# Kernel optimization log

Hardware: AMD Instinct MI355X
Metric: run time of the kernel (lower is better)

Reference implementation:

```python
import jax, jax.numpy as jnp
import numpy as np
import math

B, TT, TS, C, H, L = 8, 256, 512, 512, 8, 10
HD = C // H
TOPK_FRAME = 64
# layer schedule mirrors MultimodalTransformer.forward tower order:
# 4 stimulus cross-attn (kv=frames, topk), 2 causal self-attn, 2 history cross-attn, 2 causal self-attn
# kv_source: 0=frames, 1=self, 2=id_prev
SCHED = [(0, False, TOPK_FRAME)] * 4 + [(1, True, None)] * 2 + [(2, False, None)] * 2 + [(1, True, None)] * 2


def setup_inputs() -> dict:
    key = jax.random.key(0)
    ks = jax.random.split(key, 4)
    kws = jax.random.split(ks[3], 6)
    w = lambda k, s: jax.random.normal(k, s, jnp.float32) * 0.02
    return {
        "id_x": jax.random.normal(ks[0], (B, TT, C), jnp.float32),
        "id_prev": jax.random.normal(ks[1], (B, TT, C), jnp.float32),
        "frames": jax.random.normal(ks[2], (B, TS, C), jnp.float32),
        "Wq": w(kws[0], (L, C, C)), "bq": jnp.zeros((L, C), jnp.float32),
        "Wk": w(kws[1], (L, C, C)), "bk": jnp.zeros((L, C), jnp.float32),
        "Wv": w(kws[2], (L, C, C)), "bv": jnp.zeros((L, C), jnp.float32),
        "Wo": w(kws[3], (L, C, C)), "bo": jnp.zeros((L, C), jnp.float32),
        "W1": w(kws[4], (L, C, 4 * C)), "b1": jnp.zeros((L, 4 * C), jnp.float32),
        "W2": w(kws[5], (L, 4 * C, C)), "b2": jnp.zeros((L, C), jnp.float32),
        "ln1_g": jnp.ones((L, C), jnp.float32), "ln1_b": jnp.zeros((L, C), jnp.float32),
        "ln2_g": jnp.ones((L, C), jnp.float32), "ln2_b": jnp.zeros((L, C), jnp.float32),
        "lnf_g": jnp.ones((L, C), jnp.float32), "lnf_b": jnp.zeros((L, C), jnp.float32),
    }


def _ln(x, g, b):
    mu = x.mean(-1, keepdims=True)
    var = ((x - mu) ** 2).mean(-1, keepdims=True)
    return (x - mu) * jax.lax.rsqrt(var + 1e-5) * g + b


def _block(x, kv, causal, topk, p):
    # Block.forward: x = x + attn(ln1(x), kv, kv, mask); x = x + mlp(ln2(x)); return ln_f(x)
    Wq, bq, Wk, bk, Wv, bv, Wo, bo, W1, b1, W2, b2, l1g, l1b, l2g, l2b, lfg, lfb = p
    Bx, Tt, Cx = x.shape
    Ts = kv.shape[1]
    h = _ln(x, l1g, l1b)
    q = (h @ Wq + bq).reshape(Bx, Tt, H, HD).transpose(0, 2, 1, 3)   # [B,H,Tt,HD]
    k = (kv @ Wk + bk).reshape(Bx, Ts, H, HD).transpose(0, 2, 1, 3)  # [B,H,Ts,HD]
    v = (kv @ Wv + bv).reshape(Bx, Ts, H, HD).transpose(0, 2, 1, 3)
    att = jnp.einsum('bhqd,bhkd->bhqk', q, k) * (1.0 / math.sqrt(HD))
    if causal:
        m = jnp.tril(jnp.ones((Tt, Ts), dtype=bool))
        att = jnp.where(m, att, -jnp.inf)
    if topk is not None and topk < Ts:
        top = jax.lax.top_k(att, topk)[0]           # [B,H,Tt,topk]
        att = jnp.where(att < top[..., -1:], -jnp.inf, att)
    w_att = jax.nn.softmax(att, axis=-1)
    y = jnp.einsum('bhqk,bhkd->bhqd', w_att, v).transpose(0, 2, 1, 3).reshape(Bx, Tt, Cx)
    x = x + y @ Wo + bo
    h2 = _ln(x, l2g, l2b)
    x = x + jax.nn.gelu(h2 @ W1 + b1, approximate=False) @ W2 + b2
    return _ln(x, lfg, lfb)


def _forward(id_x, id_prev, frames, Wq, bq, Wk, bk, Wv, bv, Wo, bo, W1, b1, W2, b2,
             ln1_g, ln1_b, ln2_g, ln2_b, lnf_g, lnf_b):
    x = id_x
    for i, (src, causal, topk) in enumerate(SCHED):
        kv = (frames, x, id_prev)[src]
        p = (Wq[i], bq[i], Wk[i], bk[i], Wv[i], bv[i], Wo[i], bo[i],
             W1[i], b1[i], W2[i], b2[i],
             ln1_g[i], ln1_b[i], ln2_g[i], ln2_b[i], lnf_g[i], lnf_b[i])
        x = _block(x, kv, causal, topk, p)
    return x


def reference(id_x, id_prev, frames, Wq, bq, Wk, bk, Wv, bv, Wo, bo, W1, b1, W2, b2,
              ln1_g, ln1_b, ln2_g, ln2_b, lnf_g, lnf_b):
    return _forward(id_x, id_prev, frames, Wq, bq, Wk, bk, Wv, bv, Wo, bo, W1, b1, W2, b2,
                    ln1_g, ln1_b, ln2_g, ln2_b, lnf_g, lnf_b)
```

## Files before the change

kernel.cpp:

```cpp
#include <hip/hip_runtime.h>
#include <math.h>

#define CC 512
#define NH 8
#define HD 64
#define TT 256

typedef __attribute__((ext_vector_type(8))) short short8v;
typedef __attribute__((ext_vector_type(4))) float f32x4;

__device__ inline unsigned short bfc(float f) {
  unsigned u = __float_as_uint(f);
  return (unsigned short)((u + 0x7fffu + ((u >> 16) & 1u)) >> 16);
}
__device__ inline float b2f(unsigned short s) {
  return __uint_as_float((unsigned)s << 16);
}

__global__ __launch_bounds__(256) void prep_k(const float* __restrict__ id_x,
    const float* __restrict__ frames, const float* __restrict__ id_prev,
    float* __restrict__ x, unsigned short* __restrict__ fb,
    unsigned short* __restrict__ pb) {
  int i = blockIdx.x * 256 + threadIdx.x;
  if (i < 262144) {
    ((float4*)x)[i] = ((const float4*)id_x)[i];
  } else if (i < 786432) {
    int j = i - 262144;
    float4 f = ((const float4*)frames)[j];
    ushort4 o; o.x = bfc(f.x); o.y = bfc(f.y); o.z = bfc(f.z); o.w = bfc(f.w);
    ((ushort4*)fb)[j] = o;
  } else {
    int j = i - 786432;
    float4 f = ((const float4*)id_prev)[j];
    ushort4 o; o.x = bfc(f.x); o.y = bfc(f.y); o.z = bfc(f.z); o.w = bfc(f.w);
    ((ushort4*)pb)[j] = o;
  }
}

__global__ __launch_bounds__(256) void ln_bf(const float* __restrict__ in,
    unsigned short* __restrict__ out, const float* __restrict__ g, const float* __restrict__ b) {
  int row = blockIdx.x, t = threadIdx.x;
  const float* r = in + (size_t)row * CC;
  float v0 = r[t], v1 = r[t + 256];
  float s = v0 + v1;
  #pragma unroll
  for (int o = 32; o; o >>= 1) s += __shfl_xor(s, o);
  __shared__ float r1[4], r2[4];
  if ((t & 63) == 0) r1[t >> 6] = s;
  __syncthreads();
  float mu = (r1[0] + r1[1] + r1[2] + r1[3]) * (1.0f / CC);
  float d0 = v0 - mu, d1 = v1 - mu;
  float sq = d0 * d0 + d1 * d1;
  #pragma unroll
  for (int o = 32; o; o >>= 1) sq += __shfl_xor(sq, o);
  if ((t & 63) == 0) r2[t >> 6] = sq;
  __syncthreads();
  float inv = rsqrtf((r2[0] + r2[1] + r2[2] + r2[3]) * (1.0f / CC) + 1e-5f);
  out[(size_t)row * CC + t]       = bfc(d0 * inv * g[t] + b[t]);
  out[(size_t)row * CC + t + 256] = bfc(d1 * inv * g[t + 256] + b[t + 256]);
}

__global__ __launch_bounds__(256) void ln_final(const float* __restrict__ in,
    float* __restrict__ out, const float* __restrict__ g, const float* __restrict__ b) {
  int row = blockIdx.x, t = threadIdx.x;
  const float* r = in + (size_t)row * CC;
  float v0 = r[t], v1 = r[t + 256];
  float s = v0 + v1;
  #pragma unroll
  for (int o = 32; o; o >>= 1) s += __shfl_xor(s, o);
  __shared__ float r1[4], r2[4];
  if ((t & 63) == 0) r1[t >> 6] = s;
  __syncthreads();
  float mu = (r1[0] + r1[1] + r1[2] + r1[3]) * (1.0f / CC);
  float d0 = v0 - mu, d1 = v1 - mu;
  float sq = d0 * d0 + d1 * d1;
  #pragma unroll
  for (int o = 32; o; o >>= 1) sq += __shfl_xor(sq, o);
  if ((t & 63) == 0) r2[t >> 6] = sq;
  __syncthreads();
  float inv = rsqrtf((r2[0] + r2[1] + r2[2] + r2[3]) * (1.0f / CC) + 1e-5f);
  out[(size_t)row * CC + t]       = d0 * inv * g[t] + b[t];
  out[(size_t)row * CC + t + 256] = d1 * inv * g[t + 256] + b[t + 256];
}

__global__ __launch_bounds__(256) void ln_chain(const float* __restrict__ in,
    float* __restrict__ xout, unsigned short* __restrict__ xb,
    const float* __restrict__ gf, const float* __restrict__ bf,
    const float* __restrict__ g1, const float* __restrict__ b1,
    unsigned short* __restrict__ hout) {
  int row = blockIdx.x, t = threadIdx.x;
  const float* r = in + (size_t)row * CC;
  float v0 = r[t], v1 = r[t + 256];
  float s = v0 + v1;
  #pragma unroll
  for (int o = 32; o; o >>= 1) s += __shfl_xor(s, o);
  __shared__ float r1[4], r2[4];
  if ((t & 63) == 0) r1[t >> 6] = s;
  __syncthreads();
  float mu = (r1[0] + r1[1] + r1[2] + r1[3]) * (1.0f / CC);
  float d0 = v0 - mu, d1 = v1 - mu;
  float sq = d0 * d0 + d1 * d1;
  #pragma unroll
  for (int o = 32; o; o >>= 1) sq += __shfl_xor(sq, o);
  if ((t & 63) == 0) r2[t >> 6] = sq;
  __syncthreads();
  float inv = rsqrtf((r2[0] + r2[1] + r2[2] + r2[3]) * (1.0f / CC) + 1e-5f);
  float xf0 = d0 * inv * gf[t] + bf[t];
  float xf1 = d1 * inv * gf[t + 256] + bf[t + 256];
  xout[(size_t)row * CC + t]       = xf0;
  xout[(size_t)row * CC + t + 256] = xf1;
  xb[(size_t)row * CC + t]         = bfc(xf0);
  xb[(size_t)row * CC + t + 256]   = bfc(xf1);
  __syncthreads();
  float s2 = xf0 + xf1;
  #pragma unroll
  for (int o = 32; o; o >>= 1) s2 += __shfl_xor(s2, o);
  if ((t & 63) == 0) r1[t >> 6] = s2;
  __syncthreads();
  float mu2 = (r1[0] + r1[1] + r1[2] + r1[3]) * (1.0f / CC);
  float e0 = xf0 - mu2, e1 = xf1 - mu2;
  float sq2 = e0 * e0 + e1 * e1;
  #pragma unroll
  for (int o = 32; o; o >>= 1) sq2 += __shfl_xor(sq2, o);
  if ((t & 63) == 0) r2[t >> 6] = sq2;
  __syncthreads();
  float inv2 = rsqrtf((r2[0] + r2[1] + r2[2] + r2[3]) * (1.0f / CC) + 1e-5f);
  hout[(size_t)row * CC + t]       = bfc(e0 * inv2 * g1[t] + b1[t]);
  hout[(size_t)row * CC + t + 256] = bfc(e1 * inv2 * g1[t + 256] + b1[t + 256]);
}

__global__ __launch_bounds__(256) void transpose_w(
    const float* __restrict__ Wq, const float* __restrict__ Wk,
    const float* __restrict__ Wv, const float* __restrict__ Wo,
    const float* __restrict__ W1, const float* __restrict__ W2,
    int layer_base, unsigned short* __restrict__ wT) {
  int lz = blockIdx.x / 3072;
  int layer = layer_base + lz;
  int bid = blockIdx.x - lz * 3072;
  unsigned short* wTl = wT + (size_t)lz * 3145728;
  const float* src; unsigned short* dst; int R, Cn, tile, lg;
  if (bid < 1024) {
    int seg = bid >> 8; tile = bid & 255; R = 512; Cn = 512; lg = 4;
    const float* s4[4] = {Wq, Wk, Wv, Wo};
    src = s4[seg] + (size_t)layer * 262144;
    dst = wTl + (size_t)seg * 262144;
  } else if (bid < 2048) {
    tile = bid - 1024; R = 512; Cn = 2048; lg = 6;
    src = W1 + (size_t)layer * 1048576; dst = wTl + 1048576;
  } else {
    tile = bid - 2048; R = 2048; Cn = 512; lg = 4;
    src = W2 + (size_t)layer * 1048576; dst = wTl + 2097152;
  }
  int trb = tile >> lg, tcb = tile & ((1 << lg) - 1);
  __shared__ float tl[32][33];
  int t = threadIdx.x;
  int r = t >> 3, c4 = (t & 7) << 2;
  const float* sp = src + (size_t)(trb * 32 + r) * Cn + tcb * 32 + c4;
  float4 fv = *(const float4*)sp;
  tl[r][c4] = fv.x; tl[r][c4 + 1] = fv.y; tl[r][c4 + 2] = fv.z; tl[r][c4 + 3] = fv.w;
  __syncthreads();
  unsigned short* dp = dst + (size_t)(tcb * 32 + r) * R + trb * 32 + c4;
  ushort4 ov;
  ov.x = bfc(tl[c4][r]); ov.y = bfc(tl[c4 + 1][r]);
  ov.z = bfc(tl[c4 + 2][r]); ov.w = bfc(tl[c4 + 3][r]);
  *(ushort4*)dp = ov;
}

template<int BM, int GELU, int RES, int OUTBF, int BIAS2>
__global__ __launch_bounds__(256) void gemm_bf(
    const unsigned short* __restrict__ A, const unsigned short* __restrict__ WT,
    const float* __restrict__ bias, const float* __restrict__ bias2,
    void* __restrict__ outp, const float* __restrict__ res, int M, int N, int K) {
  __shared__ unsigned short As[BM * 64];
  __shared__ unsigned short Bs[64 * 64];
  const int tid = threadIdx.x, lane = tid & 63, wid = tid >> 6;
  const int bm = blockIdx.y * BM, bn = blockIdx.x << 6;
  const int wm = (wid >> 1) * (BM / 2), wn = (wid & 1) << 5;
  constexpr int MF = BM / 32;
  f32x4 acc[MF][2] = {};
  const int fr = lane & 15, fq = lane >> 4;
  for (int k0 = 0; k0 < K; k0 += 64) {
    if (k0) __syncthreads();
    #pragma unroll
    for (int i = 0; i < BM / 32; i++) {
      int gl = tid + (i << 8);
      int row = gl >> 3, gc = gl & 7;
      short8v d = *(const short8v*)(A + (size_t)(bm + row) * K + k0 + (gc << 3));
      *(short8v*)((char*)As + ((((row << 7) + (gc << 4))) ^ ((row & 7) << 4))) = d;
    }
    #pragma unroll
    for (int i = 0; i < 2; i++) {
      int gl = tid + (i << 8);
      int row = gl >> 3, gc = gl & 7;
      short8v d = *(const short8v*)(WT + (size_t)(bn + row) * K + k0 + (gc << 3));
      *(short8v*)((char*)Bs + ((((row << 7) + (gc << 4))) ^ ((row & 7) << 4))) = d;
    }
    __syncthreads();
    short8v af[MF][2], bf2[2][2];
    #pragma unroll
    for (int mf = 0; mf < MF; mf++)
      #pragma unroll
      for (int ks = 0; ks < 2; ks++) {
        int r = wm + mf * 16 + fr;
        int c = (ks << 2) + fq;
        af[mf][ks] = *(const short8v*)((const char*)As + ((((r << 7) + (c << 4))) ^ ((r & 7) << 4)));
      }
    #pragma unroll
    for (int nf = 0; nf < 2; nf++)
      #pragma unroll
      for (int ks = 0; ks < 2; ks++) {
        int r = wn + nf * 16 + fr;
        int c = (ks << 2) + fq;
        bf2[nf][ks] = *(const short8v*)((const char*)Bs + ((((r << 7) + (c << 4))) ^ ((r & 7) << 4)));
      }
    #pragma unroll
    for (int mf = 0; mf < MF; mf++)
      #pragma unroll
      for (int nf = 0; nf < 2; nf++) {
        acc[mf][nf] = __builtin_amdgcn_mfma_f32_16x16x32_bf16(af[mf][0], bf2[nf][0], acc[mf][nf], 0, 0, 0);
        acc[mf][nf] = __builtin_amdgcn_mfma_f32_16x16x32_bf16(af[mf][1], bf2[nf][1], acc[mf][nf], 0, 0, 0);
      }
  }
  #pragma unroll
  for (int mf = 0; mf < MF; mf++)
    #pragma unroll
    for (int nf = 0; nf < 2; nf++) {
      int col = bn + wn + nf * 16 + fr;
      float bia = (BIAS2 && col >= 512) ? bias2[col - 512] : bias[col];
      #pragma unroll
      for (int rr = 0; rr < 4; rr++) {
        int row = bm + wm + mf * 16 + fq * 4 + rr;
        float vv = acc[mf][nf][rr] + bia;
        if (GELU) vv = 0.5f * vv * (1.0f + erff(vv * 0.70710678118654752f));
        if (RES)  vv += res[(size_t)row * N + col];
        if (OUTBF) ((unsigned short*)outp)[(size_t)row * N + col] = bfc(vv);
        else       ((float*)outp)[(size_t)row * N + col] = vv;
      }
    }
}

template<int CAUSAL, int TOPK, int TSK>
__global__ __launch_bounds__(256, 5) void attn_m(
    const float* __restrict__ qf, const unsigned short* __restrict__ kv,
    unsigned short* __restrict__ yb) {
  constexpr int NT = TSK / 64;
  constexpr int NKC = TSK / 128;
  constexpr int SST = TSK + 8;
  __shared__ float S[4 * SST];
  __shared__ unsigned short Ks[128 * 64];
  __shared__ unsigned short Qs[16 * 64];
  __shared__ float swt[TOPK ? 4 : 1][TOPK ? 128 : 1];
  __shared__ unsigned short kidx[TOPK ? 4 : 1][TOPK ? 128 : 1];
  int tid = threadIdx.x, lane = tid & 63, wid = tid >> 6;
  int bid = blockIdx.x;
  int swz = ((bid & 7) << 9) | (bid >> 3);
  int b = swz >> 9, h = (swz >> 6) & 7, qt = swz & 63;
  int q0 = qt << 2;
  {
    int row = tid >> 4, c4 = (tid & 15) << 2;
    ushort4 o;
    if (row < 4) {
      float4 qv = *(const float4*)(qf + (size_t)((b << 8) + q0 + row) * CC + (h << 6) + c4);
      o.x = bfc(qv.x * 0.125f); o.y = bfc(qv.y * 0.125f);
      o.z = bfc(qv.z * 0.125f); o.w = bfc(qv.w * 0.125f);
    } else {
      o.x = o.y = o.z = o.w = 0;
    }
    int off = (row << 7) + (c4 << 1);
    *(ushort4*)((char*)Qs + (off ^ ((row & 7) << 4))) = o;
  }
  __syncthreads();
  short8v aF[2];
  {
    int r = lane & 15, kq = lane >> 4;
    #pragma unroll
    for (int kc2 = 0; kc2 < 2; kc2++)
      aF[kc2] = *(const short8v*)((const char*)Qs +
                 (((r << 7) + (kc2 << 6) + (kq << 4)) ^ ((r & 7) << 4)));
  }
  int nte = NKC;
  if (CAUSAL) { int ub = (q0 + 4 + 127) >> 7; nte = ub < NKC ? ub : NKC; }
  const unsigned short* kgb = kv + (size_t)b * TSK * 1024 + (h << 6);
  for (int t = 0; t < nte; t++) {
    __syncthreads();
    {
      int row = tid & 127, seg = tid >> 7;
      const unsigned short* src = kgb + (size_t)((t << 7) + row) * 1024 + (seg << 5);
      #pragma unroll
      for (int j = 0; j < 4; j++) {
        short8v d = *(const short8v*)(src + (j << 3));
        int slot = (seg << 2) + j;
        *(short8v*)((char*)Ks + (((row << 7) + (slot << 4)) ^ ((row & 7) << 4))) = d;
      }
    }
    __syncthreads();
    int kq = lane >> 4;
    #pragma unroll
    for (int f = 0; f < 2; f++) {
      f32x4 acc = {};
      int key16 = (wid << 5) + (f << 4) + (lane & 15);
      #pragma unroll
      for (int kc2 = 0; kc2 < 2; kc2++) {
        short8v bF = *(const short8v*)((const char*)Ks +
                      (((key16 << 7) + (kc2 << 6) + (kq << 4)) ^ ((key16 & 7) << 4)));
        acc = __builtin_amdgcn_mfma_f32_16x16x32_bf16(aF[kc2], bF, acc, 0, 0, 0);
      }
      if (kq == 0) {
        int col = (t << 7) + key16;
        #pragma unroll
        for (int r = 0; r < 4; r++)
          S[r * SST + col] = acc[r];
      }
    }
  }
  __syncthreads();
  int row = wid;
  int qi = q0 + row;
  int jmax = CAUSAL ? (qi + 1) : TSK;
  const unsigned short* vgb = kv + (size_t)b * TSK * 1024 + 512 + (h << 6) + lane;
  float sc[NT];
  float lmax = -3.0e38f;
  #pragma unroll
  for (int tt = 0; tt < NT; tt++) {
    int key = lane + (tt << 6);
    float v = (!CAUSAL || key < jmax) ? S[row * SST + key] : -3.0e38f;
    sc[tt] = v;
    lmax = fmaxf(lmax, v);
  }
  float mx = lmax;
  #pragma unroll
  for (int o = 32; o; o >>= 1) mx = fmaxf(mx, __shfl_xor(mx, o));
  float oacc = 0.f;
  if (TOPK) {
    unsigned key[NT];
    #pragma unroll
    for (int tt = 0; tt < NT; tt++) {
      unsigned u = __float_as_uint(sc[tt]);
      key[tt] = (u & 0x80000000u) ? ~u : (u | 0x80000000u);
    }
    unsigned prefix = 0u;
    #pragma unroll
    for (int bit = 31; bit >= 0; bit--) {
      unsigned cand = prefix | (1u << bit);
      int cnt = 0;
      #pragma unroll
      for (int tt = 0; tt < NT; tt++)
        cnt += __popcll(__ballot(key[tt] >= cand));
      if (cnt >= 64) prefix = cand;
    }
    float wvv[NT];
    float psum = 0.f;
    int basec = 0;
    #pragma unroll
    for (int tt = 0; tt < NT; tt++) {
      bool keep = key[tt] >= prefix;
      float wv = keep ? exp2f((sc[tt] - mx) * 1.4426950408889634f) : 0.f;
      wvv[tt] = wv;
      psum += wv;
      unsigned long long mask = __ballot(keep);
      if (keep) {
        int pos = basec + (int)__popcll(mask & ((1ull << lane) - 1ull));
        if (pos < 128) {
          kidx[row][pos] = (unsigned short)(lane + (tt << 6));
          swt[row][pos] = wv;
        }
      }
      basec += (int)__popcll(mask);
    }
    #pragma unroll
    for (int o = 32; o; o >>= 1) psum += __shfl_xor(psum, o);
    float inv = 1.0f / psum;
    int nk = basec;
    if (nk <= 128) {
      float a0 = 0.f, a1 = 0.f, a2 = 0.f, a3 = 0.f;
      int i = 0;
      for (; i + 3 < nk; i += 4) {
        a0 += swt[row][i]     * b2f(vgb[(size_t)kidx[row][i] * 1024]);
        a1 += swt[row][i + 1] * b2f(vgb[(size_t)kidx[row][i + 1] * 1024]);
        a2 += swt[row][i + 2] * b2f(vgb[(size_t)kidx[row][i + 2] * 1024]);
        a3 += swt[row][i + 3] * b2f(vgb[(size_t)kidx[row][i + 3] * 1024]);
      }
      for (; i < nk; i++) a0 += swt[row][i] * b2f(vgb[(size_t)kidx[row][i] * 1024]);
      oacc = (a0 + a1 + a2 + a3) * inv;
    } else {
      #pragma unroll
      for (int tt = 0; tt < NT; tt++)
        S[row * SST + lane + (tt << 6)] = wvv[tt];
      float a0 = 0.f, a1 = 0.f;
      for (int j = 0; j + 1 < TSK; j += 2) {
        a0 += S[row * SST + j]     * b2f(vgb[(size_t)j * 1024]);
        a1 += S[row * SST + j + 1] * b2f(vgb[(size_t)(j + 1) * 1024]);
      }
      oacc = (a0 + a1) * inv;
    }
  } else {
    float psum = 0.f;
    #pragma unroll
    for (int tt = 0; tt < NT; tt++) {
      int keyj = lane + (tt << 6);
      float wv = (keyj < jmax) ? exp2f((sc[tt] - mx) * 1.4426950408889634f) : 0.f;
      S[row * SST + keyj] = wv;
      psum += wv;
    }
    #pragma unroll
    for (int o = 32; o; o >>= 1) psum += __shfl_xor(psum, o);
    float inv = 1.0f / psum;
    float a0 = 0.f, a1 = 0.f, a2 = 0.f, a3 = 0.f;
    int j = 0;
    for (; j + 3 < jmax; j += 4) {
      a0 += S[row * SST + j]     * b2f(vgb[(size_t)j * 1024]);
      a1 += S[row * SST + j + 1] * b2f(vgb[(size_t)(j + 1) * 1024]);
      a2 += S[row * SST + j + 2] * b2f(vgb[(size_t)(j + 2) * 1024]);
      a3 += S[row * SST + j + 3] * b2f(vgb[(size_t)(j + 3) * 1024]);
    }
    for (; j < jmax; j++) a0 += S[row * SST + j] * b2f(vgb[(size_t)j * 1024]);
    oacc = (a0 + a1 + a2 + a3) * inv;
  }
  yb[(size_t)((b << 8) + qi) * CC + (h << 6) + lane] = bfc(oacc);
}

extern "C" void kernel_launch(void* const* d_in, const int* in_sizes, int n_in,
                              void* d_out, int out_size, void* d_ws, size_t ws_size,
                              hipStream_t stream) {
  const float* id_x    = (const float*)d_in[0];
  const float* id_prev = (const float*)d_in[1];
  const float* frames  = (const float*)d_in[2];
  const float* Wq = (const float*)d_in[3];  const float* bq = (const float*)d_in[4];
  const float* Wk = (const float*)d_in[5];  const float* bk = (const float*)d_in[6];
  const float* Wv = (const float*)d_in[7];  const float* bv = (const float*)d_in[8];
  const float* Wo = (const float*)d_in[9];  const float* bo = (const float*)d_in[10];
  const float* W1 = (const float*)d_in[11]; const float* b1 = (const float*)d_in[12];
  const float* W2 = (const float*)d_in[13]; const float* b2 = (const float*)d_in[14];
  const float* l1g = (const float*)d_in[15]; const float* l1b = (const float*)d_in[16];
  const float* l2g = (const float*)d_in[17]; const float* l2b = (const float*)d_in[18];
  const float* lfg = (const float*)d_in[19]; const float* lfb = (const float*)d_in[20];

  float* x = (float*)d_out;
  char* W  = (char*)d_ws;
  float*          qfb  = (float*)W;
  unsigned short* kvb  = (unsigned short*)(W + ((size_t)4  << 20));
  unsigned short* m1b  = (unsigned short*)(W + ((size_t)4  << 20));
  unsigned short* hb   = (unsigned short*)(W + ((size_t)12 << 20));
  unsigned short* ybf  = (unsigned short*)(W + ((size_t)14 << 20));
  unsigned short* xb   = (unsigned short*)(W + ((size_t)16 << 20));
  unsigned short* fb   = (unsigned short*)(W + ((size_t)18 << 20));
  unsigned short* pb   = (unsigned short*)(W + ((size_t)22 << 20));
  unsigned short* wT   = (unsigned short*)(W + ((size_t)24 << 20));

  const bool allw = ws_size >= (((size_t)24 << 20) + (size_t)10 * 3145728 * 2);

  prep_k<<<4096, 256, 0, stream>>>(id_x, frames, id_prev, x, fb, pb);
  if (allw)
    transpose_w<<<30720, 256, 0, stream>>>(Wq, Wk, Wv, Wo, W1, W2, 0, wT);

  static const int ssrc[10] = {0, 0, 0, 0, 1, 1, 2, 2, 1, 1};

  for (int i = 0; i < 10; i++) {
    if (!allw)
      transpose_w<<<3072, 256, 0, stream>>>(Wq, Wk, Wv, Wo, W1, W2, i, wT);
    unsigned short* wTl = wT + (allw ? (size_t)i * 3145728 : 0);
    unsigned short* wqT = wTl;
    unsigned short* wkvT = wTl + 262144;
    unsigned short* woT = wTl + 786432;
    unsigned short* w1T = wTl + 1048576;
    unsigned short* w2T = wTl + 2097152;

    if (i == 0)
      ln_bf<<<2048, 256, 0, stream>>>(x, hb, l1g, l1b);

    gemm_bf<32, 0, 0, 0, 0><<<dim3(8, 64), 256, 0, stream>>>(hb, wqT, bq + i * 512, nullptr, qfb, nullptr, 2048, 512, 512);

    const unsigned short* kvsrc; int Mkv;
    if (ssrc[i] == 0)      { kvsrc = fb; Mkv = 4096; }
    else if (ssrc[i] == 1) { kvsrc = xb; Mkv = 2048; }
    else                   { kvsrc = pb; Mkv = 2048; }
    if (Mkv == 4096)
      gemm_bf<64, 0, 0, 1, 1><<<dim3(16, 64), 256, 0, stream>>>(kvsrc, wkvT, bk + i * 512, bv + i * 512, kvb, nullptr, 4096, 1024, 512);
    else
      gemm_bf<32, 0, 0, 1, 1><<<dim3(16, 64), 256, 0, stream>>>(kvsrc, wkvT, bk + i * 512, bv + i * 512, kvb, nullptr, 2048, 1024, 512);

    if (ssrc[i] == 0)      attn_m<0, 1, 512><<<4096, 256, 0, stream>>>(qfb, kvb, ybf);
    else if (ssrc[i] == 1) attn_m<1, 0, 256><<<4096, 256, 0, stream>>>(qfb, kvb, ybf);
    else                   attn_m<0, 0, 256><<<4096, 256, 0, stream>>>(qfb, kvb, ybf);

    gemm_bf<32, 0, 1, 0, 0><<<dim3(8, 64), 256, 0, stream>>>(ybf, woT, bo + i * 512, nullptr, x, x, 2048, 512, 512);
    ln_bf<<<2048, 256, 0, stream>>>(x, hb, l2g + i * 512, l2b + i * 512);
    gemm_bf<64, 1, 0, 1, 0><<<dim3(32, 32), 256, 0, stream>>>(hb, w1T, b1 + i * 2048, nullptr, m1b, nullptr, 2048, 2048, 512);
    gemm_bf<32, 0, 1, 0, 0><<<dim3(8, 64), 256, 0, stream>>>(m1b, w2T, b2 + i * 512, nullptr, x, x, 2048, 512, 2048);

    if (i < 9)
      ln_chain<<<2048, 256, 0, stream>>>(x, x, xb, lfg + i * 512, lfb + i * 512,
                                         l1g + (i + 1) * 512, l1b + (i + 1) * 512, hb);
    else
      ln_final<<<2048, 256, 0, stream>>>(x, x, lfg + i * 512, lfb + i * 512);
  }
}
```

Baseline: 1.187 ms.

## Use direct-to-LDS loads, wave-per-row layernorm, bf16 Q and 8-query attention blocks

LayerNorm kernels now handle one row per wavefront with float4 loads and no shared-memory reductions or barriers. The GEMM and attention K tiles are staged with global_load_lds straight into swizzled LDS instead of going through registers. Q is written as bf16, which halves that buffer's traffic. Attention blocks become 512 threads covering 8 queries, so each K tile load is shared by more queries, and the top-k radix search exits early once exactly 64 candidates are found. These changes touch many kernels at once and risk correctness in the swizzle addressing and in the rewritten attention S-row mapping.

```diff
diff --git a/kernel.cpp b/kernel.cpp
--- a/kernel.cpp
+++ b/kernel.cpp
@@ -15,6 +15,11 @@
 }
 __device__ inline float b2f(unsigned short s) {
   return __uint_as_float((unsigned)s << 16);
+}
+__device__ inline void gld16(const void* g, void* l) {
+  __builtin_amdgcn_global_load_lds(
+      (const __attribute__((address_space(1))) unsigned int*)g,
+      (__attribute__((address_space(3))) unsigned int*)l, 16, 0, 0);
 }
 
 __global__ __launch_bounds__(256) void prep_k(const float* __restrict__ id_x,
@@ -39,48 +44,56 @@
 
 __global__ __launch_bounds__(256) void ln_bf(const float* __restrict__ in,
     unsigned short* __restrict__ out, const float* __restrict__ g, const float* __restrict__ b) {
-  int row = blockIdx.x, t = threadIdx.x;
+  int row = (blockIdx.x << 2) + (threadIdx.x >> 6), lane = threadIdx.x & 63;
   const float* r = in + (size_t)row * CC;
-  float v0 = r[t], v1 = r[t + 256];
-  float s = v0 + v1;
+  float4 v0 = *(const float4*)(r + (lane << 2));
+  float4 v1 = *(const float4*)(r + 256 + (lane << 2));
+  float s = v0.x + v0.y + v0.z + v0.w + v1.x + v1.y + v1.z + v1.w;
   #pragma unroll
   for (int o = 32; o; o >>= 1) s += __shfl_xor(s, o);
-  __shared__ float r1[4], r2[4];
-  if ((t & 63) == 0) r1[t >> 6] = s;
-  __syncthreads();
-  float mu = (r1[0] + r1[1] + r1[2] + r1[3]) * (1.0f / CC);
-  float d0 = v0 - mu, d1 = v1 - mu;
-  float sq = d0 * d0 + d1 * d1;
+  float mu = s * (1.0f / CC);
+  float d0x = v0.x - mu, d0y = v0.y - mu, d0z = v0.z - mu, d0w = v0.w - mu;
+  float d1x = v1.x - mu, d1y = v1.y - mu, d1z = v1.z - mu, d1w = v1.w - mu;
+  float sq = d0x*d0x + d0y*d0y + d0z*d0z + d0w*d0w + d1x*d1x + d1y*d1y + d1z*d1z + d1w*d1w;
   #pragma unroll
   for (int o = 32; o; o >>= 1) sq += __shfl_xor(sq, o);
-  if ((t & 63) == 0) r2[t >> 6] = sq;
-  __syncthreads();
-  float inv = rsqrtf((r2[0] + r2[1] + r2[2] + r2[3]) * (1.0f / CC) + 1e-5f);
-  out[(size_t)row * CC + t]       = bfc(d0 * inv * g[t] + b[t]);
-  out[(size_t)row * CC + t + 256] = bfc(d1 * inv * g[t + 256] + b[t + 256]);
+  float inv = rsqrtf(sq * (1.0f / CC) + 1e-5f);
+  float4 g0 = *(const float4*)(g + (lane << 2)), g1 = *(const float4*)(g + 256 + (lane << 2));
+  float4 b0 = *(const float4*)(b + (lane << 2)), b1 = *(const float4*)(b + 256 + (lane << 2));
+  ushort4 o0, o1;
+  o0.x = bfc(d0x*inv*g0.x + b0.x); o0.y = bfc(d0y*inv*g0.y + b0.y);
+  o0.z = bfc(d0z*inv*g0.z + b0.z); o0.w = bfc(d0w*inv*g0.w + b0.w);
+  o1.x = bfc(d1x*inv*g1.x + b1.x); o1.y = bfc(d1y*inv*g1.y + b1.y);
+  o1.z = bfc(d1z*inv*g1.z + b1.z); o1.w = bfc(d1w*inv*g1.w + b1.w);
+  *(ushort4*)(out + (size_t)row * CC + (lane << 2)) = o0;
+  *(ushort4*)(out + (size_t)row * CC + 256 + (lane << 2)) = o1;
 }
 
 __global__ __launch_bounds__(256) void ln_final(const float* __restrict__ in,
     float* __restrict__ out, const float* __restrict__ g, const float* __restrict__ b) {
-  int row = blockIdx.x, t = threadIdx.x;
+  int row = (blockIdx.x << 2) + (threadIdx.x >> 6), lane = threadIdx.x & 63;
   const float* r = in + (size_t)row * CC;
-  float v0 = r[t], v1 = r[t + 256];
-  float s = v0 + v1;
+  float4 v0 = *(const float4*)(r + (lane << 2));
+  float4 v1 = *(const float4*)(r + 256 + (lane << 2));
+  float s = v0.x + v0.y + v0.z + v0.w + v1.x + v1.y + v1.z + v1.w;
   #pragma unroll
   for (int o = 32; o; o >>= 1) s += __shfl_xor(s, o);
-  __shared__ float r1[4], r2[4];
-  if ((t & 63) == 0) r1[t >> 6] = s;
-  __syncthreads();
-  float mu = (r1[0] + r1[1] + r1[2] + r1[3]) * (1.0f / CC);
-  float d0 = v0 - mu, d1 = v1 - mu;
-  float sq = d0 * d0 + d1 * d1;
+  float mu = s * (1.0f / CC);
+  float d0x = v0.x - mu, d0y = v0.y - mu, d0z = v0.z - mu, d0w = v0.w - mu;
+  float d1x = v1.x - mu, d1y = v1.y - mu, d1z = v1.z - mu, d1w = v1.w - mu;
+  float sq = d0x*d0x + d0y*d0y + d0z*d0z + d0w*d0w + d1x*d1x + d1y*d1y + d1z*d1z + d1w*d1w;
   #pragma unroll
   for (int o = 32; o; o >>= 1) sq += __shfl_xor(sq, o);
-  if ((t & 63) == 0) r2[t >> 6] = sq;
-  __syncthreads();
-  float inv = rsqrtf((r2[0] + r2[1] + r2[2] + r2[3]) * (1.0f / CC) + 1e-5f);
-  out[(size_t)row * CC + t]       = d0 * inv * g[t] + b[t];
-  out[(size_t)row * CC + t + 256] = d1 * inv * g[t + 256] + b[t + 256];
+  float inv = rsqrtf(sq * (1.0f / CC) + 1e-5f);
+  float4 g0 = *(const float4*)(g + (lane << 2)), g1 = *(const float4*)(g + 256 + (lane << 2));
+  float4 b0 = *(const float4*)(b + (lane << 2)), b1 = *(const float4*)(b + 256 + (lane << 2));
+  float4 o0, o1;
+  o0.x = d0x*inv*g0.x + b0.x; o0.y = d0y*inv*g0.y + b0.y;
+  o0.z = d0z*inv*g0.z + b0.z; o0.w = d0w*inv*g0.w + b0.w;
+  o1.x = d1x*inv*g1.x + b1.x; o1.y = d1y*inv*g1.y + b1.y;
+  o1.z = d1z*inv*g1.z + b1.z; o1.w = d1w*inv*g1.w + b1.w;
+  *(float4*)(out + (size_t)row * CC + (lane << 2)) = o0;
+  *(float4*)(out + (size_t)row * CC + 256 + (lane << 2)) = o1;
 }
 
 __global__ __launch_bounds__(256) void ln_chain(const float* __restrict__ in,
@@ -88,45 +101,53 @@
     const float* __restrict__ gf, const float* __restrict__ bf,
     const float* __restrict__ g1, const float* __restrict__ b1,
     unsigned short* __restrict__ hout) {
-  int row = blockIdx.x, t = threadIdx.x;
+  int row = (blockIdx.x << 2) + (threadIdx.x >> 6), lane = threadIdx.x & 63;
   const float* r = in + (size_t)row * CC;
-  float v0 = r[t], v1 = r[t + 256];
-  float s = v0 + v1;
+  float4 v0 = *(const float4*)(r + (lane << 2));
+  float4 v1 = *(const float4*)(r + 256 + (lane << 2));
+  float s = v0.x + v0.y + v0.z + v0.w + v1.x + v1.y + v1.z + v1.w;
   #pragma unroll
   for (int o = 32; o; o >>= 1) s += __shfl_xor(s, o);
-  __shared__ float r1[4], r2[4];
-  if ((t & 63) == 0) r1[t >> 6] = s;
-  __syncthreads();
-  float mu = (r1[0] + r1[1] + r1[2] + r1[3]) * (1.0f / CC);
-  float d0 = v0 - mu, d1 = v1 - mu;
-  float sq = d0 * d0 + d1 * d1;
+  float mu = s * (1.0f / CC);
+  float d0x = v0.x - mu, d0y = v0.y - mu, d0z = v0.z - mu, d0w = v0.w - mu;
+  float d1x = v1.x - mu, d1y = v1.y - mu, d1z = v1.z - mu, d1w = v1.w - mu;
+  float sq = d0x*d0x + d0y*d0y + d0z*d0z + d0w*d0w + d1x*d1x + d1y*d1y + d1z*d1z + d1w*d1w;
   #pragma unroll
   for (int o = 32; o; o >>= 1) sq += __shfl_xor(sq, o);
-  if ((t & 63) == 0) r2[t >> 6] = sq;
-  __syncthreads();
-  float inv = rsqrtf((r2[0] + r2[1] + r2[2] + r2[3]) * (1.0f / CC) + 1e-5f);
-  float xf0 = d0 * inv * gf[t] + bf[t];
-  float xf1 = d1 * inv * gf[t + 256] + bf[t + 256];
-  xout[(size_t)row * CC + t]       = xf0;
-  xout[(size_t)row * CC + t + 256] = xf1;
-  xb[(size_t)row * CC + t]         = bfc(xf0);
-  xb[(size_t)row * CC + t + 256]   = bfc(xf1);
-  __syncthreads();
-  float s2 = xf0 + xf1;
+  float inv = rsqrtf(sq * (1.0f / CC) + 1e-5f);
+  float4 g0 = *(const float4*)(gf + (lane << 2)), g1v = *(const float4*)(gf + 256 + (lane << 2));
+  float4 b0 = *(const float4*)(bf + (lane << 2)), b1v = *(const float4*)(bf + 256 + (lane << 2));
+  float4 x0, x1;
+  x0.x = d0x*inv*g0.x + b0.x; x0.y = d0y*inv*g0.y + b0.y;
+  x0.z = d0z*inv*g0.z + b0.z; x0.w = d0w*inv*g0.w + b0.w;
+  x1.x = d1x*inv*g1v.x + b1v.x; x1.y = d1y*inv*g1v.y + b1v.y;
+  x1.z = d1z*inv*g1v.z + b1v.z; x1.w = d1w*inv*g1v.w + b1v.w;
+  *(float4*)(xout + (size_t)row * CC + (lane << 2)) = x0;
+  *(float4*)(xout + (size_t)row * CC + 256 + (lane << 2)) = x1;
+  ushort4 xb0, xb1;
+  xb0.x = bfc(x0.x); xb0.y = bfc(x0.y); xb0.z = bfc(x0.z); xb0.w = bfc(x0.w);
+  xb1.x = bfc(x1.x); xb1.y = bfc(x1.y); xb1.z = bfc(x1.z); xb1.w = bfc(x1.w);
+  *(ushort4*)(xb + (size_t)row * CC + (lane << 2)) = xb0;
+  *(ushort4*)(xb + (size_t)row * CC + 256 + (lane << 2)) = xb1;
+  float s2 = x0.x + x0.y + x0.z + x0.w + x1.x + x1.y + x1.z + x1.w;
   #pragma unroll
   for (int o = 32; o; o >>= 1) s2 += __shfl_xor(s2, o);
-  if ((t & 63) == 0) r1[t >> 6] = s2;
-  __syncthreads();
-  float mu2 = (r1[0] + r1[1] + r1[2] + r1[3]) * (1.0f / CC);
-  float e0 = xf0 - mu2, e1 = xf1 - mu2;
-  float sq2 = e0 * e0 + e1 * e1;
+  float mu2 = s2 * (1.0f / CC);
+  float e0x = x0.x - mu2, e0y = x0.y - mu2, e0z = x0.z - mu2, e0w = x0.w - mu2;
+  float e1x = x1.x - mu2, e1y = x1.y - mu2, e1z = x1.z - mu2, e1w = x1.w - mu2;
+  float sq2 = e0x*e0x + e0y*e0y + e0z*e0z + e0w*e0w + e1x*e1x + e1y*e1y + e1z*e1z + e1w*e1w;
   #pragma unroll
   for (int o = 32; o; o >>= 1) sq2 += __shfl_xor(sq2, o);
-  if ((t & 63) == 0) r2[t >> 6] = sq2;
-  __syncthreads();
-  float inv2 = rsqrtf((r2[0] + r2[1] + r2[2] + r2[3]) * (1.0f / CC) + 1e-5f);
-  hout[(size_t)row * CC + t]       = bfc(e0 * inv2 * g1[t] + b1[t]);
-  hout[(size_t)row * CC + t + 256] = bfc(e1 * inv2 * g1[t + 256] + b1[t + 256]);
+  float inv2 = rsqrtf(sq2 * (1.0f / CC) + 1e-5f);
+  float4 h0 = *(const float4*)(g1 + (lane << 2)), h1 = *(const float4*)(g1 + 256 + (lane << 2));
+  float4 c0 = *(const float4*)(b1 + (lane << 2)), c1 = *(const float4*)(b1 + 256 + (lane << 2));
+  ushort4 ho0, ho1;
+  ho0.x = bfc(e0x*inv2*h0.x + c0.x); ho0.y = bfc(e0y*inv2*h0.y + c0.y);
+  ho0.z = bfc(e0z*inv2*h0.z + c0.z); ho0.w = bfc(e0w*inv2*h0.w + c0.w);
+  ho1.x = bfc(e1x*inv2*h1.x + c1.x); ho1.y = bfc(e1y*inv2*h1.y + c1.y);
+  ho1.z = bfc(e1z*inv2*h1.z + c1.z); ho1.w = bfc(e1w*inv2*h1.w + c1.w);
+  *(ushort4*)(hout + (size_t)row * CC + (lane << 2)) = ho0;
+  *(ushort4*)(hout + (size_t)row * CC + 256 + (lane << 2)) = ho1;
 }
 
 __global__ __launch_bounds__(256) void transpose_w(
@@ -171,8 +192,8 @@
     const unsigned short* __restrict__ A, const unsigned short* __restrict__ WT,
     const float* __restrict__ bias, const float* __restrict__ bias2,
     void* __restrict__ outp, const float* __restrict__ res, int M, int N, int K) {
-  __shared__ unsigned short As[BM * 64];
-  __shared__ unsigned short Bs[64 * 64];
+  __shared__ __align__(16) unsigned short As[BM * 64];
+  __shared__ __align__(16) unsigned short Bs[64 * 64];
   const int tid = threadIdx.x, lane = tid & 63, wid = tid >> 6;
   const int bm = blockIdx.y * BM, bn = blockIdx.x << 6;
   const int wm = (wid >> 1) * (BM / 2), wn = (wid & 1) << 5;
@@ -185,15 +206,17 @@
     for (int i = 0; i < BM / 32; i++) {
       int gl = tid + (i << 8);
       int row = gl >> 3, gc = gl & 7;
-      short8v d = *(const short8v*)(A + (size_t)(bm + row) * K + k0 + (gc << 3));
-      *(short8v*)((char*)As + ((((row << 7) + (gc << 4))) ^ ((row & 7) << 4))) = d;
+      int gcs = gc ^ (row & 7);
+      gld16(A + (size_t)(bm + row) * K + k0 + (gcs << 3),
+            (char*)As + (i << 12) + (wid << 10));
     }
     #pragma unroll
     for (int i = 0; i < 2; i++) {
       int gl = tid + (i << 8);
       int row = gl >> 3, gc = gl & 7;
-      short8v d = *(const short8v*)(WT + (size_t)(bn + row) * K + k0 + (gc << 3));
-      *(short8v*)((char*)Bs + ((((row << 7) + (gc << 4))) ^ ((row & 7) << 4))) = d;
+      int gcs = gc ^ (row & 7);
+      gld16(WT + (size_t)(bn + row) * K + k0 + (gcs << 3),
+            (char*)Bs + (i << 12) + (wid << 10));
     }
     __syncthreads();
     short8v af[MF][2], bf2[2][2];
@@ -240,77 +263,69 @@
 }
 
 template<int CAUSAL, int TOPK, int TSK>
-__global__ __launch_bounds__(256, 5) void attn_m(
-    const float* __restrict__ qf, const unsigned short* __restrict__ kv,
+__global__ __launch_bounds__(512, 4) void attn_m(
+    const unsigned short* __restrict__ qb, const unsigned short* __restrict__ kv,
     unsigned short* __restrict__ yb) {
   constexpr int NT = TSK / 64;
   constexpr int NKC = TSK / 128;
   constexpr int SST = TSK + 8;
-  __shared__ float S[4 * SST];
-  __shared__ unsigned short Ks[128 * 64];
-  __shared__ unsigned short Qs[16 * 64];
-  __shared__ float swt[TOPK ? 4 : 1][TOPK ? 128 : 1];
-  __shared__ unsigned short kidx[TOPK ? 4 : 1][TOPK ? 128 : 1];
+  __shared__ float S[8 * SST];
+  __shared__ __align__(16) unsigned short Ks[128 * 64];
+  __shared__ __align__(16) unsigned short Qs[16 * 64];
+  __shared__ float swt[TOPK ? 8 : 1][TOPK ? 128 : 1];
+  __shared__ unsigned short kidx[TOPK ? 8 : 1][TOPK ? 128 : 1];
   int tid = threadIdx.x, lane = tid & 63, wid = tid >> 6;
   int bid = blockIdx.x;
-  int swz = ((bid & 7) << 9) | (bid >> 3);
-  int b = swz >> 9, h = (swz >> 6) & 7, qt = swz & 63;
-  int q0 = qt << 2;
-  {
-    int row = tid >> 4, c4 = (tid & 15) << 2;
-    ushort4 o;
-    if (row < 4) {
-      float4 qv = *(const float4*)(qf + (size_t)((b << 8) + q0 + row) * CC + (h << 6) + c4);
-      o.x = bfc(qv.x * 0.125f); o.y = bfc(qv.y * 0.125f);
-      o.z = bfc(qv.z * 0.125f); o.w = bfc(qv.w * 0.125f);
-    } else {
-      o.x = o.y = o.z = o.w = 0;
-    }
-    int off = (row << 7) + (c4 << 1);
-    *(ushort4*)((char*)Qs + (off ^ ((row & 7) << 4))) = o;
+  int swz = ((bid & 7) << 8) | (bid >> 3);
+  int b = swz >> 8, h = (swz >> 5) & 7, q0 = (swz & 31) << 3;
+  if (tid < 128) {
+    int row = tid >> 3, gc = tid & 7;
+    short8v o8 = {0, 0, 0, 0, 0, 0, 0, 0};
+    if (row < 8) {
+      const unsigned short* qsrc = qb + (size_t)((b << 8) + q0 + row) * CC + (h << 6) + (gc << 3);
+      short8v raw = *(const short8v*)qsrc;
+      #pragma unroll
+      for (int e = 0; e < 8; e++)
+        o8[e] = (short)bfc(b2f((unsigned short)raw[e]) * 0.125f);
+    }
+    *(short8v*)((char*)Qs + ((tid << 4) ^ ((row & 7) << 4))) = o8;
   }
   __syncthreads();
   short8v aF[2];
   {
-    int r = lane & 15, kq = lane >> 4;
+    int r = lane & 15, kq2 = lane >> 4;
     #pragma unroll
     for (int kc2 = 0; kc2 < 2; kc2++)
       aF[kc2] = *(const short8v*)((const char*)Qs +
-                 (((r << 7) + (kc2 << 6) + (kq << 4)) ^ ((r & 7) << 4)));
+                 (((r << 7) + (kc2 << 6) + (kq2 << 4)) ^ ((r & 7) << 4)));
   }
   int nte = NKC;
-  if (CAUSAL) { int ub = (q0 + 4 + 127) >> 7; nte = ub < NKC ? ub : NKC; }
+  if (CAUSAL) { int ub = (q0 + 8 + 127) >> 7; nte = ub < NKC ? ub : NKC; }
   const unsigned short* kgb = kv + (size_t)b * TSK * 1024 + (h << 6);
   for (int t = 0; t < nte; t++) {
     __syncthreads();
-    {
-      int row = tid & 127, seg = tid >> 7;
-      const unsigned short* src = kgb + (size_t)((t << 7) + row) * 1024 + (seg << 5);
-      #pragma unroll
-      for (int j = 0; j < 4; j++) {
-        short8v d = *(const short8v*)(src + (j << 3));
-        int slot = (seg << 2) + j;
-        *(short8v*)((char*)Ks + (((row << 7) + (slot << 4)) ^ ((row & 7) << 4))) = d;
-      }
+    #pragma unroll
+    for (int j = 0; j < 2; j++) {
+      int s = (wid << 7) + (j << 6) + lane;
+      int row = s >> 3, sp = s & 7;
+      gld16(kgb + (size_t)((t << 7) + row) * 1024 + ((sp ^ (row & 7)) << 3),
+            (char*)Ks + (wid << 11) + (j << 10));
     }
     __syncthreads();
-    int kq = lane >> 4;
-    #pragma unroll
-    for (int f = 0; f < 2; f++) {
-      f32x4 acc = {};
-      int key16 = (wid << 5) + (f << 4) + (lane & 15);
-      #pragma unroll
-      for (int kc2 = 0; kc2 < 2; kc2++) {
-        short8v bF = *(const short8v*)((const char*)Ks +
-                      (((key16 << 7) + (kc2 << 6) + (kq << 4)) ^ ((key16 & 7) << 4)));
-        acc = __builtin_amdgcn_mfma_f32_16x16x32_bf16(aF[kc2], bF, acc, 0, 0, 0);
-      }
-      if (kq == 0) {
-        int col = (t << 7) + key16;
-        #pragma unroll
-        for (int r = 0; r < 4; r++)
-          S[r * SST + col] = acc[r];
-      }
+    int kq2 = lane >> 4;
+    f32x4 acc = {};
+    int key16 = (wid << 4) + (lane & 15);
+    #pragma unroll
+    for (int kc2 = 0; kc2 < 2; kc2++) {
+      short8v bF = *(const short8v*)((const char*)Ks +
+                    (((key16 << 7) + (kc2 << 6) + (kq2 << 4)) ^ ((key16 & 7) << 4)));
+      acc = __builtin_amdgcn_mfma_f32_16x16x32_bf16(aF[kc2], bF, acc, 0, 0, 0);
+    }
+    if (kq2 < 2) {
+      int col = (t << 7) + key16;
+      #pragma unroll
+      for (int r = 0; r < 4; r++)
+        S[(kq2 * 4 + r) * SST + col] = acc[r];
     }
   }
   __syncthreads();
@@ -339,14 +354,16 @@
       key[tt] = (u & 0x80000000u) ? ~u : (u | 0x80000000u);
     }
     unsigned prefix = 0u;
-    #pragma unroll
     for (int bit = 31; bit >= 0; bit--) {
       unsigned cand = prefix | (1u << bit);
       int cnt = 0;
       #pragma unroll
       for (int tt = 0; tt < NT; tt++)
         cnt += __popcll(__ballot(key[tt] >= cand));
-      if (cnt >= 64) prefix = cand;
+      if (cnt >= 64) {
+        prefix = cand;
+        if (cnt == 64) break;
+      }
     }
     float wvv[NT];
     float psum = 0.f;
@@ -437,7 +454,7 @@
 
   float* x = (float*)d_out;
   char* W  = (char*)d_ws;
-  float*          qfb  = (float*)W;
+  unsigned short* qbuf = (unsigned short*)W;
   unsigned short* kvb  = (unsigned short*)(W + ((size_t)4  << 20));
   unsigned short* m1b  = (unsigned short*)(W + ((size_t)4  << 20));
   unsigned short* hb   = (unsigned short*)(W + ((size_t)12 << 20));
@@ -466,9 +483,9 @@
     unsigned short* w2T = wTl + 2097152;
 
     if (i == 0)
-      ln_bf<<<2048, 256, 0, stream>>>(x, hb, l1g, l1b);
-
-    gemm_bf<32, 0, 0, 0, 0><<<dim3(8, 64), 256, 0, stream>>>(hb, wqT, bq + i * 512, nullptr, qfb, nullptr, 2048, 512, 512);
+      ln_bf<<<512, 256, 0, stream>>>(x, hb, l1g, l1b);
+
+    gemm_bf<32, 0, 0, 1, 0><<<dim3(8, 64), 256, 0, stream>>>(hb, wqT, bq + i * 512, nullptr, qbuf, nullptr, 2048, 512, 512);
 
     const unsigned short* kvsrc; int Mkv;
     if (ssrc[i] == 0)      { kvsrc = fb; Mkv = 4096; }
@@ -479,19 +496,19 @@
     else
       gemm_bf<32, 0, 0, 1, 1><<<dim3(16, 64), 256, 0, stream>>>(kvsrc, wkvT, bk + i * 512, bv + i * 512, kvb, nullptr, 2048, 1024, 512);
 
-    if (ssrc[i] == 0)      attn_m<0, 1, 512><<<4096, 256, 0, stream>>>(qfb, kvb, ybf);
-    else if (ssrc[i] == 1) attn_m<1, 0, 256><<<4096, 256, 0, stream>>>(qfb, kvb, ybf);
-    else                   attn_m<0, 0, 256><<<4096, 256, 0, stream>>>(qfb, kvb, ybf);
+    if (ssrc[i] == 0)      attn_m<0, 1, 512><<<2048, 512, 0, stream>>>(qbuf, kvb, ybf);
+    else if (ssrc[i] == 1) attn_m<1, 0, 256><<<2048, 512, 0, stream>>>(qbuf, kvb, ybf);
+    else                   attn_m<0, 0, 256><<<2048, 512, 0, stream>>>(qbuf, kvb, ybf);
 
     gemm_bf<32, 0, 1, 0, 0><<<dim3(8, 64), 256, 0, stream>>>(ybf, woT, bo + i * 512, nullptr, x, x, 2048, 512, 512);
-    ln_bf<<<2048, 256, 0, stream>>>(x, hb, l2g + i * 512, l2b + i * 512);
+    ln_bf<<<512, 256, 0, stream>>>(x, hb, l2g + i * 512, l2b + i * 512);
     gemm_bf<64, 1, 0, 1, 0><<<dim3(32, 32), 256, 0, stream>>>(hb, w1T, b1 + i * 2048, nullptr, m1b, nullptr, 2048, 2048, 512);
     gemm_bf<32, 0, 1, 0, 0><<<dim3(8, 64), 256, 0, stream>>>(m1b, w2T, b2 + i * 512, nullptr, x, x, 2048, 512, 2048);
 
     if (i < 9)
-      ln_chain<<<2048, 256, 0, stream>>>(x, x, xb, lfg + i * 512, lfb + i * 512,
-                                         l1g + (i + 1) * 512, l1b + (i + 1) * 512, hb);
+      ln_chain<<<512, 256, 0, stream>>>(x, x, xb, lfg + i * 512, lfb + i * 512,
+                                        l1g + (i + 1) * 512, l1b + (i + 1) * 512, hb);
     else
-      ln_final<<<2048, 256, 0, stream>>>(x, x, lfg + i * 512, lfb + i * 512);
-  }
-}
+      ln_final<<<512, 256, 0, stream>>>(x, x, lfg + i * 512, lfb + i * 512);
+  }
+}
```

After: 1.006 ms. -15.2%, faster.
